# Kernel optimization log

Hardware: AMD Instinct MI355X
Metric: run time of the kernel (lower is better)

## Reference

```python
import jax, jax.numpy as jnp
import numpy as np

D_MODEL = 1024
NUM_HEADS = 16
DEPTH = D_MODEL // NUM_HEADS
B, S = 2, 2048


def setup_inputs() -> dict:
    key = jax.random.key(0)
    ks = jax.random.split(key, 12)
    scale = 1.0 / np.sqrt(D_MODEL)
    inp = {
        "Q": jax.random.normal(ks[0], (B, S, D_MODEL), jnp.float32),
        "K": jax.random.normal(ks[1], (B, S, D_MODEL), jnp.float32),
        "V": jax.random.normal(ks[2], (B, S, D_MODEL), jnp.float32),
        "mask": jnp.zeros((B, 1, 1, S), jnp.float32),  # 1.0 = masked, 0.0 = attend
        "Wq": jax.random.normal(ks[3], (D_MODEL, D_MODEL), jnp.float32) * scale,
        "bq": jnp.zeros((D_MODEL,), jnp.float32),
        "Wk": jax.random.normal(ks[4], (D_MODEL, D_MODEL), jnp.float32) * scale,
        "bk": jnp.zeros((D_MODEL,), jnp.float32),
        "Wv": jax.random.normal(ks[5], (D_MODEL, D_MODEL), jnp.float32) * scale,
        "bv": jnp.zeros((D_MODEL,), jnp.float32),
        "Wo": jax.random.normal(ks[6], (D_MODEL, D_MODEL), jnp.float32) * scale,
        "bo": jnp.zeros((D_MODEL,), jnp.float32),
    }
    return inp


def _split_heads(x):
    b, s, _ = x.shape
    return x.reshape(b, s, NUM_HEADS, DEPTH).transpose(0, 2, 1, 3)  # [b,h,s,d]


def reference(Q, K, V, mask, Wq, bq, Wk, bk, Wv, bv, Wo, bo):
    q = _split_heads(Q @ Wq + bq)
    k = _split_heads(K @ Wk + bk)
    v = _split_heads(V @ Wv + bv)
    scores = jnp.einsum("bhqd,bhkd->bhqk", q, k) / jnp.sqrt(jnp.float32(DEPTH))
    scores = scores + mask * -1e9
    attn = jax.nn.softmax(scores, axis=-1)  # [b,h,q,k]
    out = jnp.einsum("bhqk,bhkd->bhqd", attn, v)
    out = out.transpose(0, 2, 1, 3).reshape(Q.shape[0], -1, D_MODEL)
    out = out @ Wo + bo
    return out, attn
```

## Files before the change

### kernel.cpp

```cpp
#include <hip/hip_runtime.h>

#define D_MODEL 1024
#define NHEADS  16
#define DEPTH   64
#define BB      2
#define SS      2048
#define MROWS   (BB*SS)
#define BHN     (BB*NHEADS)

using f16 = _Float16;
using f16x4 = __attribute__((ext_vector_type(4))) _Float16;
using f16x8 = __attribute__((ext_vector_type(8))) _Float16;
using f32x4 = __attribute__((ext_vector_type(4))) float;

__device__ __forceinline__ void g2l16(const void* g, void* l) {
  __builtin_amdgcn_global_load_lds(
      (const __attribute__((address_space(1))) void*)g,
      (__attribute__((address_space(3))) void*)l, 16, 0, 0);
}

__global__ __launch_bounds__(256) void wtrans(
    const float* __restrict__ w0, const float* __restrict__ w1,
    const float* __restrict__ w2, const float* __restrict__ w3,
    f16* __restrict__ wt) {
  const float* W = blockIdx.z == 0 ? w0 : blockIdx.z == 1 ? w1 : blockIdx.z == 2 ? w2 : w3;
  f16* Wt = wt + (size_t)blockIdx.z * D_MODEL * D_MODEL;
  __shared__ float tile[64][65];
  const int t = threadIdx.x;
  const int bx = blockIdx.x * 64, by = blockIdx.y * 64;
  const int c = t & 63, r0 = t >> 6;
#pragma unroll
  for (int i = 0; i < 16; ++i) {
    int r = r0 + i * 4;
    tile[r][c] = W[(size_t)(by + r) * D_MODEL + bx + c];
  }
  __syncthreads();
#pragma unroll
  for (int i = 0; i < 16; ++i) {
    int r = r0 + i * 4;
    Wt[(size_t)(bx + r) * D_MODEL + by + c] = (f16)tile[c][r];
  }
}

__global__ __launch_bounds__(256) void proj_gemm(
    const float* __restrict__ Q, const float* __restrict__ K, const float* __restrict__ V,
    const f16* __restrict__ Wt,
    const float* __restrict__ bq, const float* __restrict__ bk, const float* __restrict__ bv,
    f16* __restrict__ heads) {
  const int z = blockIdx.z;
  const float* A = z == 0 ? Q : z == 1 ? K : V;
  const f16* Bt = Wt + (size_t)z * D_MODEL * D_MODEL;
  const float* bias = z == 0 ? bq : z == 1 ? bk : bv;
  f16* dst = heads + (size_t)z * MROWS * D_MODEL;

  __shared__ f16 As[128 * 32];
  __shared__ f16 Bs[128 * 32];
  const int t = threadIdx.x, lane = t & 63, w = t >> 6;
  const int m0 = blockIdx.y * 128, n0 = blockIdx.x * 128;
  const int wr = (w >> 1) * 64, wc = (w & 1) * 64;
  f32x4 acc[4][4] = {};

  for (int k0 = 0; k0 < D_MODEL; k0 += 32) {
    __syncthreads();
#pragma unroll
    for (int i = 0; i < 4; ++i) {
      int f = t + i * 256;
      int row = f >> 3, c4 = (f & 7) * 4;
      const float4 v4 = *(const float4*)(A + (size_t)(m0 + row) * D_MODEL + k0 + c4);
      f16* p = &As[row * 32 + c4];
      p[0] = (f16)v4.x; p[1] = (f16)v4.y; p[2] = (f16)v4.z; p[3] = (f16)v4.w;
    }
#pragma unroll
    for (int i = 0; i < 2; ++i) {
      int seg = t + i * 256;
      int row = seg >> 2, c8 = (seg & 3) * 8;
      g2l16(Bt + (size_t)(n0 + row) * D_MODEL + k0 + c8, &Bs[seg * 8]);
    }
    __syncthreads();
    f16x8 af[4], bfr[4];
#pragma unroll
    for (int i = 0; i < 4; ++i)
      af[i] = *(const f16x8*)&As[(wr + i * 16 + (lane & 15)) * 32 + (lane >> 4) * 8];
#pragma unroll
    for (int j = 0; j < 4; ++j)
      bfr[j] = *(const f16x8*)&Bs[(wc + j * 16 + (lane & 15)) * 32 + (lane >> 4) * 8];
#pragma unroll
    for (int i = 0; i < 4; ++i)
#pragma unroll
      for (int j = 0; j < 4; ++j)
        acc[i][j] = __builtin_amdgcn_mfma_f32_16x16x32_f16(af[i], bfr[j], acc[i][j], 0, 0, 0);
  }
#pragma unroll
  for (int i = 0; i < 4; ++i)
#pragma unroll
    for (int j = 0; j < 4; ++j) {
      int n = n0 + wc + j * 16 + (lane & 15);
      float bn = bias[n];
      int h = n >> 6, d = n & 63;
#pragma unroll
      for (int r = 0; r < 4; ++r) {
        int m = m0 + wr + i * 16 + (lane >> 4) * 4 + r;
        int b = m >> 11, s = m & 2047;
        dst[((size_t)(b * NHEADS + h) * SS + s) * DEPTH + d] = (f16)(acc[i][j][r] + bn);
      }
    }
}

__global__ __launch_bounds__(256) void vtrans(
    const f16* __restrict__ vh, f16* __restrict__ vt) {
  const int bh = blockIdx.y;
  const int n0 = blockIdx.x * 128;
  const f16* src = vh + (size_t)bh * SS * DEPTH;
  f16* dst = vt + (size_t)bh * DEPTH * SS;
  __shared__ f16 tile[128][72];
  const int t = threadIdx.x;
#pragma unroll
  for (int iss = 0; iss < 4; ++iss) {
    int seg = t + iss * 256;
    int n = seg >> 3, c = seg & 7;
    *(f16x8*)&tile[n][c * 8] = *(const f16x8*)(src + (size_t)(n0 + n) * DEPTH + c * 8);
  }
  __syncthreads();
#pragma unroll
  for (int iss = 0; iss < 4; ++iss) {
    int seg = t + iss * 256;
    int d = seg >> 4, c = seg & 15;
    f16x8 v;
#pragma unroll
    for (int e = 0; e < 8; ++e) v[e] = tile[c * 8 + e][d];
    *(f16x8*)(dst + (size_t)d * SS + n0 + c * 8) = v;
  }
}

__global__ __launch_bounds__(256) void attn_fused(
    const f16* __restrict__ qh, const f16* __restrict__ kh,
    const f16* __restrict__ vt, const float* __restrict__ mask,
    float* __restrict__ attn, f16* __restrict__ outh) {
  const int bh = blockIdx.y, b = bh >> 4, h = bh & 15;
  const int m0 = blockIdx.x * 128;
  const f16* Kb = kh + (size_t)bh * SS * DEPTH;
  const f16* Vb = vt + (size_t)bh * DEPTH * SS;
  const float* mB = mask + (size_t)b * SS;
  float* Ab = attn + (size_t)bh * SS * SS;

  __shared__ f16 Ks[2][128 * 64];
  __shared__ f16 Vs[2][64 * 128];

  const int t = threadIdx.x, lane = t & 63, w = t >> 6;
  const int l15 = lane & 15, g = lane >> 4;

  f16x8 bq[2][2];
  {
    const f16* Qb = qh + (size_t)bh * SS * DEPTH;
#pragma unroll
    for (int j = 0; j < 2; ++j)
#pragma unroll
      for (int kk = 0; kk < 2; ++kk)
        bq[j][kk] = *(const f16x8*)(Qb + (size_t)(m0 + w * 32 + j * 16 + l15) * DEPTH + kk * 32 + g * 8);
  }

  auto stageK = [&](int buf, int ct) {
#pragma unroll
    for (int iss = 0; iss < 4; ++iss) {
      int seg = t + iss * 256;
      int n = seg >> 3, c = seg & 7;
      int csrc = c ^ (n & 7);
      g2l16(Kb + (size_t)(ct * 128 + n) * DEPTH + csrc * 8, &Ks[buf][seg * 8]);
    }
  };
  auto stageV = [&](int buf, int ct) {
#pragma unroll
    for (int iss = 0; iss < 4; ++iss) {
      int seg = t + iss * 256;
      int d = seg >> 4, c = seg & 15;
      int csrc = c ^ ((d >> 1) & 7);
      g2l16(Vb + (size_t)d * SS + ct * 128 + csrc * 8, &Vs[buf][seg * 8]);
    }
  };
  auto qkStep = [&](const f16* ks, f32x4 (&accS)[8][2]) {
#pragma unroll
    for (int kk = 0; kk < 2; ++kk) {
#pragma unroll
      for (int i = 0; i < 8; ++i) {
        int n = i * 16 + l15;
        int c = (g + 4 * kk) ^ (l15 & 7);
        f16x8 ak = *(const f16x8*)&ks[n * 64 + c * 8];
#pragma unroll
        for (int j = 0; j < 2; ++j)
          accS[i][j] = __builtin_amdgcn_mfma_f32_16x16x32_f16(ak, bq[j][kk], accS[i][j], 0, 0, 0);
      }
    }
  };

  float rm[2] = {-3.0e38f, -3.0e38f}, rs[2] = {0.0f, 0.0f};
  stageK(0, 0);
  __syncthreads();
  for (int ct = 0; ct < 16; ++ct) {
    const int cur = ct & 1;
    if (ct < 15) stageK(cur ^ 1, ct + 1);
    f32x4 accS[8][2] = {};
    qkStep(Ks[cur], accS);
#pragma unroll
    for (int i = 0; i < 8; ++i) {
      const float4 m4 = *(const float4*)(mB + ct * 128 + i * 16 + g * 4);
      const float mv[4] = {m4.x * -1e9f, m4.y * -1e9f, m4.z * -1e9f, m4.w * -1e9f};
#pragma unroll
      for (int j = 0; j < 2; ++j)
#pragma unroll
        for (int r = 0; r < 4; ++r)
          accS[i][j][r] = accS[i][j][r] * 0.125f + mv[r];
    }
#pragma unroll
    for (int j = 0; j < 2; ++j) {
      float tm = -3.0e38f;
#pragma unroll
      for (int i = 0; i < 8; ++i)
        tm = fmaxf(tm, fmaxf(fmaxf(accS[i][j][0], accS[i][j][1]),
                             fmaxf(accS[i][j][2], accS[i][j][3])));
      tm = fmaxf(tm, __shfl_xor(tm, 16, 64));
      tm = fmaxf(tm, __shfl_xor(tm, 32, 64));
      const float mn = fmaxf(rm[j], tm);
      float ts = 0.0f;
#pragma unroll
      for (int i = 0; i < 8; ++i)
#pragma unroll
        for (int r = 0; r < 4; ++r)
          ts += __expf(accS[i][j][r] - mn);
      ts += __shfl_xor(ts, 16, 64);
      ts += __shfl_xor(ts, 32, 64);
      rs[j] = rs[j] * __expf(rm[j] - mn) + ts;
      rm[j] = mn;
    }
    __syncthreads();
  }

  const float invs[2] = {1.0f / rs[0], 1.0f / rs[1]};
  f32x4 accO[2][4] = {};
  stageK(0, 0); stageV(0, 0);
  __syncthreads();
  for (int ct = 0; ct < 16; ++ct) {
    const int cur = ct & 1;
    if (ct < 15) { stageK(cur ^ 1, ct + 1); stageV(cur ^ 1, ct + 1); }
    f32x4 accS[8][2] = {};
    qkStep(Ks[cur], accS);
    const f16* vs = Vs[cur];
#pragma unroll
    for (int i = 0; i < 8; ++i) {
      const float4 m4 = *(const float4*)(mB + ct * 128 + i * 16 + g * 4);
      const float mv[4] = {m4.x * -1e9f, m4.y * -1e9f, m4.z * -1e9f, m4.w * -1e9f};
      f16x4 bv[4];
#pragma unroll
      for (int df = 0; df < 4; ++df) {
        const int d = df * 16 + l15;
        const int c16 = 2 * i + (g >> 1);
        const int sw = c16 ^ ((d >> 1) & 7);
        bv[df] = *(const f16x4*)&vs[d * 128 + sw * 8 + (g & 1) * 4];
      }
#pragma unroll
      for (int j = 0; j < 2; ++j) {
        float p[4];
#pragma unroll
        for (int r = 0; r < 4; ++r)
          p[r] = __expf(accS[i][j][r] * 0.125f + mv[r] - rm[j]) * invs[j];
        float4 st; st.x = p[0]; st.y = p[1]; st.z = p[2]; st.w = p[3];
        *(float4*)(Ab + (size_t)(m0 + w * 32 + j * 16 + l15) * SS + ct * 128 + i * 16 + g * 4) = st;
        f16x4 pa; pa[0] = (f16)p[0]; pa[1] = (f16)p[1]; pa[2] = (f16)p[2]; pa[3] = (f16)p[3];
#pragma unroll
        for (int df = 0; df < 4; ++df)
          accO[j][df] = __builtin_amdgcn_mfma_f32_16x16x16f16(pa, bv[df], accO[j][df], 0, 0, 0);
      }
    }
    __syncthreads();
  }

  f16* Ob = outh + (size_t)b * SS * D_MODEL + h * DEPTH;
#pragma unroll
  for (int j = 0; j < 2; ++j)
#pragma unroll
    for (int df = 0; df < 4; ++df) {
      const int d = df * 16 + l15;
#pragma unroll
      for (int r = 0; r < 4; ++r) {
        const int s = m0 + w * 32 + j * 16 + g * 4 + r;
        Ob[(size_t)s * D_MODEL + d] = (f16)accO[j][df][r];
      }
    }
}

__global__ __launch_bounds__(256) void final_gemm(
    const f16* __restrict__ A, const f16* __restrict__ Bt,
    const float* __restrict__ bias, float* __restrict__ out) {
  __shared__ f16 As[128 * 32];
  __shared__ f16 Bs[128 * 32];
  const int t = threadIdx.x, lane = t & 63, w = t >> 6;
  const int m0 = blockIdx.y * 128, n0 = blockIdx.x * 128;
  const int wr = (w >> 1) * 64, wc = (w & 1) * 64;
  f32x4 acc[4][4] = {};

  for (int k0 = 0; k0 < D_MODEL; k0 += 32) {
    __syncthreads();
#pragma unroll
    for (int i = 0; i < 2; ++i) {
      int seg = t + i * 256;
      int row = seg >> 2, c8 = (seg & 3) * 8;
      g2l16(A + (size_t)(m0 + row) * D_MODEL + k0 + c8, &As[seg * 8]);
      g2l16(Bt + (size_t)(n0 + row) * D_MODEL + k0 + c8, &Bs[seg * 8]);
    }
    __syncthreads();
    f16x8 af[4], bfr[4];
#pragma unroll
    for (int i = 0; i < 4; ++i)
      af[i] = *(const f16x8*)&As[(wr + i * 16 + (lane & 15)) * 32 + (lane >> 4) * 8];
#pragma unroll
    for (int j = 0; j < 4; ++j)
      bfr[j] = *(const f16x8*)&Bs[(wc + j * 16 + (lane & 15)) * 32 + (lane >> 4) * 8];
#pragma unroll
    for (int i = 0; i < 4; ++i)
#pragma unroll
      for (int j = 0; j < 4; ++j)
        acc[i][j] = __builtin_amdgcn_mfma_f32_16x16x32_f16(af[i], bfr[j], acc[i][j], 0, 0, 0);
  }
#pragma unroll
  for (int i = 0; i < 4; ++i)
#pragma unroll
    for (int j = 0; j < 4; ++j) {
      int n = n0 + wc + j * 16 + (lane & 15);
      float bn = bias[n];
#pragma unroll
      for (int r = 0; r < 4; ++r) {
        int m = m0 + wr + i * 16 + (lane >> 4) * 4 + r;
        out[(size_t)m * D_MODEL + n] = acc[i][j][r] + bn;
      }
    }
}

extern "C" void kernel_launch(void* const* d_in, const int* in_sizes, int n_in,
                              void* d_out, int out_size, void* d_ws, size_t ws_size,
                              hipStream_t stream) {
  const float* Q    = (const float*)d_in[0];
  const float* K    = (const float*)d_in[1];
  const float* V    = (const float*)d_in[2];
  const float* mask = (const float*)d_in[3];
  const float* Wq   = (const float*)d_in[4];
  const float* bq   = (const float*)d_in[5];
  const float* Wk   = (const float*)d_in[6];
  const float* bk   = (const float*)d_in[7];
  const float* Wv   = (const float*)d_in[8];
  const float* bv   = (const float*)d_in[9];
  const float* Wo   = (const float*)d_in[10];
  const float* bo   = (const float*)d_in[11];

  float* out0 = (float*)d_out;
  float* attn = out0 + (size_t)MROWS * D_MODEL;

  char* ws = (char*)d_ws;
  f16* Wt    = (f16*)ws;
  f16* heads = (f16*)(ws + (size_t)8 * 1024 * 1024);
  f16* outh  = (f16*)(ws + (size_t)32 * 1024 * 1024);
  f16* vtr   = (f16*)(ws + (size_t)40 * 1024 * 1024);
  f16* qh = heads;
  f16* kh = heads + (size_t)MROWS * D_MODEL;
  f16* vh = heads + (size_t)2 * MROWS * D_MODEL;

  wtrans<<<dim3(16, 16, 4), 256, 0, stream>>>(Wq, Wk, Wv, Wo, Wt);
  proj_gemm<<<dim3(8, 32, 3), 256, 0, stream>>>(Q, K, V, Wt, bq, bk, bv, heads);
  vtrans<<<dim3(16, BHN), 256, 0, stream>>>(vh, vtr);
  attn_fused<<<dim3(16, BHN), 256, 0, stream>>>(qh, kh, vtr, mask, attn, outh);
  final_gemm<<<dim3(8, 32), 256, 0, stream>>>(outh, Wt + (size_t)3 * D_MODEL * D_MODEL, bo, out0);
}
```

Baseline: 850.5 us.

## Pre-cast QKV to fp16, widen GEMM K-tile, raise MFMA priority

Adds a cast kernel that converts Q, K and V to fp16 once, staging them in the not-yet-written attention output buffer, so proj_gemm can load A tiles with direct global-to-LDS loads instead of per-thread float conversion. Both GEMMs now use a 64-wide K tile, which halves the number of barrier-separated iterations. The attention kernel wraps its MFMA blocks in s_setprio to favour matrix issue. The trade-off is an extra full read and write pass over the inputs and doubled LDS per block, which may lower occupancy.

Result: slower. 880.4 us (+3.5%).

```diff
diff --git a/kernel.cpp b/kernel.cpp
--- a/kernel.cpp
+++ b/kernel.cpp
@@ -17,6 +17,20 @@
   __builtin_amdgcn_global_load_lds(
       (const __attribute__((address_space(1))) void*)g,
       (__attribute__((address_space(3))) void*)l, 16, 0, 0);
+}
+
+__global__ __launch_bounds__(256) void cast_qkv(
+    const float* __restrict__ Q, const float* __restrict__ K,
+    const float* __restrict__ V, f16* __restrict__ dst) {
+  const float* src = blockIdx.z == 0 ? Q : blockIdx.z == 1 ? K : V;
+  f16* d = dst + (size_t)blockIdx.z * MROWS * D_MODEL;
+  const size_t i = ((size_t)blockIdx.x * 256 + threadIdx.x) * 8;
+  const float4 a = *(const float4*)(src + i);
+  const float4 b = *(const float4*)(src + i + 4);
+  f16x8 o;
+  o[0] = (f16)a.x; o[1] = (f16)a.y; o[2] = (f16)a.z; o[3] = (f16)a.w;
+  o[4] = (f16)b.x; o[5] = (f16)b.y; o[6] = (f16)b.z; o[7] = (f16)b.w;
+  *(f16x8*)(d + i) = o;
 }
 
 __global__ __launch_bounds__(256) void wtrans(
@@ -43,63 +57,59 @@
 }
 
 __global__ __launch_bounds__(256) void proj_gemm(
-    const float* __restrict__ Q, const float* __restrict__ K, const float* __restrict__ V,
-    const f16* __restrict__ Wt,
+    const f16* __restrict__ qkv16, const f16* __restrict__ Wt,
     const float* __restrict__ bq, const float* __restrict__ bk, const float* __restrict__ bv,
     f16* __restrict__ heads) {
   const int z = blockIdx.z;
-  const float* A = z == 0 ? Q : z == 1 ? K : V;
+  const f16* A = qkv16 + (size_t)z * MROWS * D_MODEL;
   const f16* Bt = Wt + (size_t)z * D_MODEL * D_MODEL;
   const float* bias = z == 0 ? bq : z == 1 ? bk : bv;
   f16* dst = heads + (size_t)z * MROWS * D_MODEL;
 
-  __shared__ f16 As[128 * 32];
-  __shared__ f16 Bs[128 * 32];
+  __shared__ f16 As[128 * 64];
+  __shared__ f16 Bs[128 * 64];
   const int t = threadIdx.x, lane = t & 63, w = t >> 6;
+  const int l15 = lane & 15, g = lane >> 4;
   const int m0 = blockIdx.y * 128, n0 = blockIdx.x * 128;
   const int wr = (w >> 1) * 64, wc = (w & 1) * 64;
   f32x4 acc[4][4] = {};
 
-  for (int k0 = 0; k0 < D_MODEL; k0 += 32) {
+  for (int k0 = 0; k0 < D_MODEL; k0 += 64) {
     __syncthreads();
 #pragma unroll
     for (int i = 0; i < 4; ++i) {
-      int f = t + i * 256;
-      int row = f >> 3, c4 = (f & 7) * 4;
-      const float4 v4 = *(const float4*)(A + (size_t)(m0 + row) * D_MODEL + k0 + c4);
-      f16* p = &As[row * 32 + c4];
-      p[0] = (f16)v4.x; p[1] = (f16)v4.y; p[2] = (f16)v4.z; p[3] = (f16)v4.w;
-    }
-#pragma unroll
-    for (int i = 0; i < 2; ++i) {
       int seg = t + i * 256;
-      int row = seg >> 2, c8 = (seg & 3) * 8;
+      int row = seg >> 3, c8 = (seg & 7) * 8;
+      g2l16(A  + (size_t)(m0 + row) * D_MODEL + k0 + c8, &As[seg * 8]);
       g2l16(Bt + (size_t)(n0 + row) * D_MODEL + k0 + c8, &Bs[seg * 8]);
     }
     __syncthreads();
-    f16x8 af[4], bfr[4];
-#pragma unroll
-    for (int i = 0; i < 4; ++i)
-      af[i] = *(const f16x8*)&As[(wr + i * 16 + (lane & 15)) * 32 + (lane >> 4) * 8];
-#pragma unroll
-    for (int j = 0; j < 4; ++j)
-      bfr[j] = *(const f16x8*)&Bs[(wc + j * 16 + (lane & 15)) * 32 + (lane >> 4) * 8];
-#pragma unroll
-    for (int i = 0; i < 4; ++i)
+#pragma unroll
+    for (int kk = 0; kk < 2; ++kk) {
+      f16x8 af[4], bfr[4];
+#pragma unroll
+      for (int i = 0; i < 4; ++i)
+        af[i] = *(const f16x8*)&As[(wr + i * 16 + l15) * 64 + kk * 32 + g * 8];
 #pragma unroll
       for (int j = 0; j < 4; ++j)
-        acc[i][j] = __builtin_amdgcn_mfma_f32_16x16x32_f16(af[i], bfr[j], acc[i][j], 0, 0, 0);
+        bfr[j] = *(const f16x8*)&Bs[(wc + j * 16 + l15) * 64 + kk * 32 + g * 8];
+#pragma unroll
+      for (int i = 0; i < 4; ++i)
+#pragma unroll
+        for (int j = 0; j < 4; ++j)
+          acc[i][j] = __builtin_amdgcn_mfma_f32_16x16x32_f16(af[i], bfr[j], acc[i][j], 0, 0, 0);
+    }
   }
 #pragma unroll
   for (int i = 0; i < 4; ++i)
 #pragma unroll
     for (int j = 0; j < 4; ++j) {
-      int n = n0 + wc + j * 16 + (lane & 15);
+      int n = n0 + wc + j * 16 + l15;
       float bn = bias[n];
       int h = n >> 6, d = n & 63;
 #pragma unroll
       for (int r = 0; r < 4; ++r) {
-        int m = m0 + wr + i * 16 + (lane >> 4) * 4 + r;
+        int m = m0 + wr + i * 16 + g * 4 + r;
         int b = m >> 11, s = m & 2047;
         dst[((size_t)(b * NHEADS + h) * SS + s) * DEPTH + d] = (f16)(acc[i][j][r] + bn);
       }
@@ -178,6 +188,7 @@
     }
   };
   auto qkStep = [&](const f16* ks, f32x4 (&accS)[8][2]) {
+    __builtin_amdgcn_s_setprio(1);
 #pragma unroll
     for (int kk = 0; kk < 2; ++kk) {
 #pragma unroll
@@ -190,6 +201,7 @@
           accS[i][j] = __builtin_amdgcn_mfma_f32_16x16x32_f16(ak, bq[j][kk], accS[i][j], 0, 0, 0);
       }
     }
+    __builtin_amdgcn_s_setprio(0);
   };
 
   float rm[2] = {-3.0e38f, -3.0e38f}, rs[2] = {0.0f, 0.0f};
@@ -265,9 +277,11 @@
         float4 st; st.x = p[0]; st.y = p[1]; st.z = p[2]; st.w = p[3];
         *(float4*)(Ab + (size_t)(m0 + w * 32 + j * 16 + l15) * SS + ct * 128 + i * 16 + g * 4) = st;
         f16x4 pa; pa[0] = (f16)p[0]; pa[1] = (f16)p[1]; pa[2] = (f16)p[2]; pa[3] = (f16)p[3];
+        __builtin_amdgcn_s_setprio(1);
 #pragma unroll
         for (int df = 0; df < 4; ++df)
           accO[j][df] = __builtin_amdgcn_mfma_f32_16x16x16f16(pa, bv[df], accO[j][df], 0, 0, 0);
+        __builtin_amdgcn_s_setprio(0);
       }
     }
     __syncthreads();
@@ -290,45 +304,49 @@
 __global__ __launch_bounds__(256) void final_gemm(
     const f16* __restrict__ A, const f16* __restrict__ Bt,
     const float* __restrict__ bias, float* __restrict__ out) {
-  __shared__ f16 As[128 * 32];
-  __shared__ f16 Bs[128 * 32];
+  __shared__ f16 As[128 * 64];
+  __shared__ f16 Bs[128 * 64];
   const int t = threadIdx.x, lane = t & 63, w = t >> 6;
+  const int l15 = lane & 15, g = lane >> 4;
   const int m0 = blockIdx.y * 128, n0 = blockIdx.x * 128;
   const int wr = (w >> 1) * 64, wc = (w & 1) * 64;
   f32x4 acc[4][4] = {};
 
-  for (int k0 = 0; k0 < D_MODEL; k0 += 32) {
-    __syncthreads();
-#pragma unroll
-    for (int i = 0; i < 2; ++i) {
+  for (int k0 = 0; k0 < D_MODEL; k0 += 64) {
+    __syncthreads();
+#pragma unroll
+    for (int i = 0; i < 4; ++i) {
       int seg = t + i * 256;
-      int row = seg >> 2, c8 = (seg & 3) * 8;
-      g2l16(A + (size_t)(m0 + row) * D_MODEL + k0 + c8, &As[seg * 8]);
+      int row = seg >> 3, c8 = (seg & 7) * 8;
+      g2l16(A  + (size_t)(m0 + row) * D_MODEL + k0 + c8, &As[seg * 8]);
       g2l16(Bt + (size_t)(n0 + row) * D_MODEL + k0 + c8, &Bs[seg * 8]);
     }
     __syncthreads();
-    f16x8 af[4], bfr[4];
-#pragma unroll
-    for (int i = 0; i < 4; ++i)
-      af[i] = *(const f16x8*)&As[(wr + i * 16 + (lane & 15)) * 32 + (lane >> 4) * 8];
-#pragma unroll
-    for (int j = 0; j < 4; ++j)
-      bfr[j] = *(const f16x8*)&Bs[(wc + j * 16 + (lane & 15)) * 32 + (lane >> 4) * 8];
-#pragma unroll
-    for (int i = 0; i < 4; ++i)
+#pragma unroll
+    for (int kk = 0; kk < 2; ++kk) {
+      f16x8 af[4], bfr[4];
+#pragma unroll
+      for (int i = 0; i < 4; ++i)
+        af[i] = *(const f16x8*)&As[(wr + i * 16 + l15) * 64 + kk * 32 + g * 8];
 #pragma unroll
       for (int j = 0; j < 4; ++j)
-        acc[i][j] = __builtin_amdgcn_mfma_f32_16x16x32_f16(af[i], bfr[j], acc[i][j], 0, 0, 0);
+        bfr[j] = *(const f16x8*)&Bs[(wc + j * 16 + l15) * 64 + kk * 32 + g * 8];
+#pragma unroll
+      for (int i = 0; i < 4; ++i)
+#pragma unroll
+        for (int j = 0; j < 4; ++j)
+          acc[i][j] = __builtin_amdgcn_mfma_f32_16x16x32_f16(af[i], bfr[j], acc[i][j], 0, 0, 0);
+    }
   }
 #pragma unroll
   for (int i = 0; i < 4; ++i)
 #pragma unroll
     for (int j = 0; j < 4; ++j) {
-      int n = n0 + wc + j * 16 + (lane & 15);
+      int n = n0 + wc + j * 16 + l15;
       float bn = bias[n];
 #pragma unroll
       for (int r = 0; r < 4; ++r) {
-        int m = m0 + wr + i * 16 + (lane >> 4) * 4 + r;
+        int m = m0 + wr + i * 16 + g * 4 + r;
         out[(size_t)m * D_MODEL + n] = acc[i][j][r] + bn;
       }
     }
@@ -362,8 +380,11 @@
   f16* kh = heads + (size_t)MROWS * D_MODEL;
   f16* vh = heads + (size_t)2 * MROWS * D_MODEL;
 
+  f16* qkv16 = (f16*)attn;
+
+  cast_qkv<<<dim3(2048, 1, 3), 256, 0, stream>>>(Q, K, V, qkv16);
   wtrans<<<dim3(16, 16, 4), 256, 0, stream>>>(Wq, Wk, Wv, Wo, Wt);
-  proj_gemm<<<dim3(8, 32, 3), 256, 0, stream>>>(Q, K, V, Wt, bq, bk, bv, heads);
+  proj_gemm<<<dim3(8, 32, 3), 256, 0, stream>>>(qkv16, Wt, bq, bk, bv, heads);
   vtrans<<<dim3(16, BHN), 256, 0, stream>>>(vh, vtr);
   attn_fused<<<dim3(16, BHN), 256, 0, stream>>>(qh, kh, vtr, mask, attn, outh);
   final_gemm<<<dim3(8, 32), 256, 0, stream>>>(outh, Wt + (size_t)3 * D_MODEL * D_MODEL, bo, out0);
```
